# Optimization experiments

Measured on AMD Instinct MI355X. Metric: run time of the kernel, lower is better.

The kernel has to match this reference:

```python
import jax, jax.numpy as jnp
import numpy as np

K = 1  # from init_kwargs; block assembly forces k == 1 (x_mean last dim is 1)


def setup_inputs() -> dict:
    key = jax.random.key(0)
    # (N, C, W, T, V, M)
    x = jax.random.normal(key, (64, 3, 16, 128, 25, 2), dtype=jnp.float32)
    return {"x": x}


def reference(x):
    N, C, W, T, V, M = x.shape
    k = K
    # permute(0,3,4,5,2,1) -> (N,T,V,M,W,C), then row-major reshape to (-1,C,W)
    # (faithful to torch .contiguous().view, which reinterprets the W*C block)
    xr = jnp.transpose(x, (0, 3, 4, 5, 2, 1)).reshape(-1, C, W)  # (B, C, W)
    x_mean = jnp.mean(xr, axis=2, keepdims=True)                  # (B, C, 1)
    x_center = xr - x_mean
    x_cov = jnp.einsum('bcw,bdw->bcd', x_center, x_center) / (W - 1)  # (B,C,C)
    tr = jnp.einsum('bii->b', x_cov)[:, None, None]               # (B,1,1)
    x_cov = x_cov / tr + tr * (jnp.eye(C, dtype=x.dtype) * 0.001)

    x_mean = x_mean.reshape(N, T, V, M, C, 1)
    x_cov = x_cov.reshape(N, T, V, M, C, C)

    det_sigma = jnp.linalg.det(x_cov)[..., None, None]            # (N,T,V,M,1,1)
    power = -1.0 / (C + k)
    det_sigma_power = det_sigma ** power

    if k == 0:
        return det_sigma_power * x_cov

    mu_outer = jnp.einsum('...ci,...di->...cd', x_mean, x_mean)   # (...,C,C)
    sigma_plus = x_cov + k * mu_outer
    mean_t = jnp.swapaxes(x_mean, -1, -2)                         # (...,k,C)
    I_k = jnp.broadcast_to(jnp.eye(k, dtype=x.dtype), (N, T, V, M, k, k))
    top = jnp.concatenate([sigma_plus, x_mean], axis=-1)          # (...,C,C+k)
    bottom = jnp.concatenate([mean_t, I_k], axis=-1)              # (...,k,C+k)
    block = jnp.concatenate([top, bottom], axis=-2)               # (...,C+k,C+k)
    return det_sigma_power * block
```

## Files before the change

### kernel.cpp

```cpp
#include <hip/hip_runtime.h>


__global__ void __launch_bounds__(256)
gaussian_embed_kernel(const float* __restrict__ x, float* __restrict__ out, int B) {
    int b = blockIdx.x * blockDim.x + threadIdx.x;
    if (b >= B) return;

    const int n   = b / 6400;
    const int rem = b - n * 6400;
    const float* __restrict__ xb = x + (size_t)n * 307200 + rem;

    float f[48];
#pragma unroll
    for (int i = 0; i < 48; ++i) {
        const int c_orig = i % 3;
        const int w_orig = i / 3;
        f[i] = xb[c_orig * 102400 + w_orig * 6400];
    }

    float m0 = 0.f, m1 = 0.f, m2 = 0.f;
#pragma unroll
    for (int w = 0; w < 16; ++w) { m0 += f[w]; m1 += f[16 + w]; m2 += f[32 + w]; }
    m0 *= (1.f / 16.f); m1 *= (1.f / 16.f); m2 *= (1.f / 16.f);

#pragma unroll
    for (int w = 0; w < 16; ++w) { f[w] -= m0; f[16 + w] -= m1; f[32 + w] -= m2; }

    float c00 = 0.f, c01 = 0.f, c02 = 0.f, c11 = 0.f, c12 = 0.f, c22 = 0.f;
#pragma unroll
    for (int w = 0; w < 16; ++w) {
        const float a = f[w], bb = f[16 + w], cc = f[32 + w];
        c00 += a * a;  c01 += a * bb; c02 += a * cc;
        c11 += bb * bb; c12 += bb * cc; c22 += cc * cc;
    }
    const float inv15 = 1.f / 15.f;
    c00 *= inv15; c01 *= inv15; c02 *= inv15;
    c11 *= inv15; c12 *= inv15; c22 *= inv15;

    const float tr    = c00 + c11 + c22;
    const float invtr = 1.f / tr;
    const float diag  = 0.001f * tr;
    const float a = c00 * invtr + diag;
    const float bq = c01 * invtr;
    const float cq = c02 * invtr;
    const float d = c11 * invtr + diag;
    const float e = c12 * invtr;
    const float g = c22 * invtr + diag;

    const float det = a * (d * g - e * e) - bq * (bq * g - cq * e) + cq * (bq * e - cq * d);
    const float dsp = powf(det, -0.25f);

    const float om01 = dsp * (bq + m0 * m1);
    const float om02 = dsp * (cq + m0 * m2);
    const float om12 = dsp * (e + m1 * m2);
    const float dm0 = dsp * m0, dm1 = dsp * m1, dm2 = dsp * m2;

    float4 r0 = make_float4(dsp * (a + m0 * m0), om01, om02, dm0);
    float4 r1 = make_float4(om01, dsp * (d + m1 * m1), om12, dm1);
    float4 r2 = make_float4(om02, om12, dsp * (g + m2 * m2), dm2);
    float4 r3 = make_float4(dm0, dm1, dm2, dsp);

    float4* __restrict__ o = (float4*)(out + (size_t)b * 16);
    o[0] = r0; o[1] = r1; o[2] = r2; o[3] = r3;
}

extern "C" void kernel_launch(void* const* d_in, const int* in_sizes, int n_in,
                              void* d_out, int out_size, void* d_ws, size_t ws_size,
                              hipStream_t stream) {
    const float* x = (const float*)d_in[0];
    float* out = (float*)d_out;
    const int B = in_sizes[0] / 48;
    const int threads = 256;
    const int blocks = (B + threads - 1) / threads;
    gaussian_embed_kernel<<<blocks, threads, 0, stream>>>(x, out, B);
}
```

Before: 24.00 us.

## Process four batch items per thread with float4 loads and single-pass moments

Each thread now handles four consecutive batch entries, loading float4 vectors along the contiguous TVM axis instead of scalar loads. The covariance is computed in one pass from sums and sums of products rather than mean-then-center, and powf is replaced by rsqrt(sqrt). This aims to cut load instruction count and register pressure from the 48-element array, at the risk of fewer threads, poorer occupancy and slightly different numerics from the one-pass variance formula.

```diff
diff --git a/kernel.cpp b/kernel.cpp
--- a/kernel.cpp
+++ b/kernel.cpp
@@ -2,66 +2,70 @@
 
 
 __global__ void __launch_bounds__(256)
-gaussian_embed_kernel(const float* __restrict__ x, float* __restrict__ out, int B) {
-    int b = blockIdx.x * blockDim.x + threadIdx.x;
-    if (b >= B) return;
-
+gaussian_embed_kernel(const float* __restrict__ x, float* __restrict__ out, int B4) {
+    int t = blockIdx.x * blockDim.x + threadIdx.x;
+    if (t >= B4) return;
+    const int b   = t << 2;
     const int n   = b / 6400;
     const int rem = b - n * 6400;
-    const float* __restrict__ xb = x + (size_t)n * 307200 + rem;
+    const float4* __restrict__ xb = (const float4*)(x + (size_t)n * 307200 + rem);
 
-    float f[48];
+    float s0[4] = {0,0,0,0}, s1[4] = {0,0,0,0}, s2[4] = {0,0,0,0};
+    float p00[4] = {0,0,0,0}, p01[4] = {0,0,0,0}, p02[4] = {0,0,0,0};
+    float p11[4] = {0,0,0,0}, p12[4] = {0,0,0,0}, p22[4] = {0,0,0,0};
+
 #pragma unroll
-    for (int i = 0; i < 48; ++i) {
-        const int c_orig = i % 3;
-        const int w_orig = i / 3;
-        f[i] = xb[c_orig * 102400 + w_orig * 6400];
+    for (int w = 0; w < 16; ++w) {
+        const int i0 = w, i1 = w + 16, i2 = w + 32;
+        const float4 av = xb[(i0 % 3) * 25600 + (i0 / 3) * 1600];
+        const float4 bv = xb[(i1 % 3) * 25600 + (i1 / 3) * 1600];
+        const float4 cv = xb[(i2 % 3) * 25600 + (i2 / 3) * 1600];
+        const float a[4]  = {av.x, av.y, av.z, av.w};
+        const float bb[4] = {bv.x, bv.y, bv.z, bv.w};
+        const float cc[4] = {cv.x, cv.y, cv.z, cv.w};
+#pragma unroll
+        for (int j = 0; j < 4; ++j) {
+            s0[j]  += a[j];          s1[j]  += bb[j];          s2[j]  += cc[j];
+            p00[j] += a[j] * a[j];   p01[j] += a[j] * bb[j];   p02[j] += a[j] * cc[j];
+            p11[j] += bb[j] * bb[j]; p12[j] += bb[j] * cc[j];  p22[j] += cc[j] * cc[j];
+        }
     }
 
-    float m0 = 0.f, m1 = 0.f, m2 = 0.f;
 #pragma unroll
-    for (int w = 0; w < 16; ++w) { m0 += f[w]; m1 += f[16 + w]; m2 += f[32 + w]; }
-    m0 *= (1.f / 16.f); m1 *= (1.f / 16.f); m2 *= (1.f / 16.f);
+    for (int j = 0; j < 4; ++j) {
+        const float m0 = s0[j] * 0.0625f, m1 = s1[j] * 0.0625f, m2 = s2[j] * 0.0625f;
+        const float inv15 = 1.f / 15.f;
+        const float c00 = (p00[j] - 16.f * m0 * m0) * inv15;
+        const float c01 = (p01[j] - 16.f * m0 * m1) * inv15;
+        const float c02 = (p02[j] - 16.f * m0 * m2) * inv15;
+        const float c11 = (p11[j] - 16.f * m1 * m1) * inv15;
+        const float c12 = (p12[j] - 16.f * m1 * m2) * inv15;
+        const float c22 = (p22[j] - 16.f * m2 * m2) * inv15;
 
-#pragma unroll
-    for (int w = 0; w < 16; ++w) { f[w] -= m0; f[16 + w] -= m1; f[32 + w] -= m2; }
+        const float tr    = c00 + c11 + c22;
+        const float invtr = 1.f / tr;
+        const float diag  = 0.001f * tr;
+        const float a  = c00 * invtr + diag;
+        const float bq = c01 * invtr;
+        const float cq = c02 * invtr;
+        const float d  = c11 * invtr + diag;
+        const float e  = c12 * invtr;
+        const float g  = c22 * invtr + diag;
 
-    float c00 = 0.f, c01 = 0.f, c02 = 0.f, c11 = 0.f, c12 = 0.f, c22 = 0.f;
-#pragma unroll
-    for (int w = 0; w < 16; ++w) {
-        const float a = f[w], bb = f[16 + w], cc = f[32 + w];
-        c00 += a * a;  c01 += a * bb; c02 += a * cc;
-        c11 += bb * bb; c12 += bb * cc; c22 += cc * cc;
+        const float det = a * (d * g - e * e) - bq * (bq * g - cq * e) + cq * (bq * e - cq * d);
+        const float dsp = rsqrtf(sqrtf(det));
+
+        const float om01 = dsp * (bq + m0 * m1);
+        const float om02 = dsp * (cq + m0 * m2);
+        const float om12 = dsp * (e + m1 * m2);
+        const float dm0 = dsp * m0, dm1 = dsp * m1, dm2 = dsp * m2;
+
+        float4* __restrict__ o = (float4*)(out + (size_t)(b + j) * 16);
+        o[0] = make_float4(dsp * (a + m0 * m0), om01, om02, dm0);
+        o[1] = make_float4(om01, dsp * (d + m1 * m1), om12, dm1);
+        o[2] = make_float4(om02, om12, dsp * (g + m2 * m2), dm2);
+        o[3] = make_float4(dm0, dm1, dm2, dsp);
     }
-    const float inv15 = 1.f / 15.f;
-    c00 *= inv15; c01 *= inv15; c02 *= inv15;
-    c11 *= inv15; c12 *= inv15; c22 *= inv15;
-
-    const float tr    = c00 + c11 + c22;
-    const float invtr = 1.f / tr;
-    const float diag  = 0.001f * tr;
-    const float a = c00 * invtr + diag;
-    const float bq = c01 * invtr;
-    const float cq = c02 * invtr;
-    const float d = c11 * invtr + diag;
-    const float e = c12 * invtr;
-    const float g = c22 * invtr + diag;
-
-    const float det = a * (d * g - e * e) - bq * (bq * g - cq * e) + cq * (bq * e - cq * d);
-    const float dsp = powf(det, -0.25f);
-
-    const float om01 = dsp * (bq + m0 * m1);
-    const float om02 = dsp * (cq + m0 * m2);
-    const float om12 = dsp * (e + m1 * m2);
-    const float dm0 = dsp * m0, dm1 = dsp * m1, dm2 = dsp * m2;
-
-    float4 r0 = make_float4(dsp * (a + m0 * m0), om01, om02, dm0);
-    float4 r1 = make_float4(om01, dsp * (d + m1 * m1), om12, dm1);
-    float4 r2 = make_float4(om02, om12, dsp * (g + m2 * m2), dm2);
-    float4 r3 = make_float4(dm0, dm1, dm2, dsp);
-
-    float4* __restrict__ o = (float4*)(out + (size_t)b * 16);
-    o[0] = r0; o[1] = r1; o[2] = r2; o[3] = r3;
 }
 
 extern "C" void kernel_launch(void* const* d_in, const int* in_sizes, int n_in,
@@ -69,8 +73,9 @@
                               hipStream_t stream) {
     const float* x = (const float*)d_in[0];
     float* out = (float*)d_out;
-    const int B = in_sizes[0] / 48;
+    const int B  = in_sizes[0] / 48;
+    const int B4 = B / 4;
     const int threads = 256;
-    const int blocks = (B + threads - 1) / threads;
-    gaussian_embed_kernel<<<blocks, threads, 0, stream>>>(x, out, B);
+    const int blocks = (B4 + threads - 1) / threads;
+    gaussian_embed_kernel<<<blocks, threads, 0, stream>>>(x, out, B4);
 }
```

Measured after the change: 26.15 us. 1.09x slower.
